# Kernel optimization log

Measured on AMD Instinct MI355X. Metric: run time of the kernel, lower is better.

The kernel has to match this reference:

```python
import jax, jax.numpy as jnp
import numpy as np

B, S, D = 2, 2048, 2048          # batch, seq_len, model_dim
H, HD, RD, L = 16, 128, 64, 512  # heads, head_dim, rope_dim, latent_dim


def _rope_cos_sin(seq_len, dim, dtype):
    inv_freq = 1.0 / (10000.0 ** (jnp.arange(0, dim, 2, dtype=jnp.float32) / dim))
    freqs = jnp.outer(jnp.arange(seq_len, dtype=jnp.float32), inv_freq)  # [S, dim/2]
    emb = jnp.concatenate([freqs, freqs], axis=-1)                        # [S, dim]
    return jnp.cos(emb).astype(dtype), jnp.sin(emb).astype(dtype)


def _rotate_half(x):
    x1, x2 = jnp.split(x, 2, axis=-1)
    return jnp.concatenate([-x2, x1], axis=-1)


def _apply_rope(q, k):
    # q, k: [B, S, H, rope_dim]
    cos, sin = _rope_cos_sin(q.shape[1], q.shape[-1], q.dtype)
    cos = cos[None, :, None, :]
    sin = sin[None, :, None, :]
    return q * cos + _rotate_half(q) * sin, k * cos + _rotate_half(k) * sin


def setup_inputs() -> dict:
    key = jax.random.key(0)
    ks = jax.random.split(key, 6)
    x = jax.random.normal(ks[0], (B, S, D), dtype=jnp.float32)
    mask = jnp.tril(jnp.ones((1, 1, S, S), dtype=jnp.bool_))  # causal
    s = lambda fan_in: 1.0 / np.sqrt(fan_in)
    w_kv_down = jax.random.normal(ks[1], (D, L), jnp.float32) * s(D)
    w_kv_up = jax.random.normal(ks[2], (L, H * (2 * HD + RD)), jnp.float32) * s(L)
    w_q_down = jax.random.normal(ks[3], (D, L), jnp.float32) * s(D)
    w_q_up = jax.random.normal(ks[4], (L, H * (HD + RD)), jnp.float32) * s(L)
    w_o = jax.random.normal(ks[5], (H * HD, D), jnp.float32) * s(H * HD)
    return dict(x=x, mask=mask, w_kv_down=w_kv_down, w_kv_up=w_kv_up,
                w_q_down=w_q_down, w_q_up=w_q_up, w_o=w_o)


def reference(x, mask, w_kv_down, w_kv_up, w_q_down, w_q_up, w_o):
    b, s, _ = x.shape
    # low-rank KV path
    kv_full = (x @ w_kv_down @ w_kv_up).reshape(b, s, H, 2 * HD + RD)
    k_content = kv_full[..., :HD]
    k_rope = kv_full[..., HD:HD + RD]
    v = kv_full[..., HD + RD:]                     # [b, s, H, HD]
    # low-rank Q path
    q_full = (x @ w_q_down @ w_q_up).reshape(b, s, H, HD + RD)
    q_content = q_full[..., :HD]
    q_rope = q_full[..., HD:]
    # partial RoPE on the rope slice only
    q_rope, k_rope = _apply_rope(q_rope, k_rope)
    q = jnp.concatenate([q_content, q_rope], axis=-1)  # [b, s, H, HD+RD]
    k = jnp.concatenate([k_content, k_rope], axis=-1)
    scale = 1.0 / np.sqrt(HD + RD)
    scores = jnp.einsum('bqhd,bkhd->bhqk', q, k) * scale
    scores = jnp.where(mask, scores, jnp.finfo(scores.dtype).min)
    attn = jax.nn.softmax(scores, axis=-1)          # dropout_p=0.0 -> identity
    context = jnp.einsum('bhqk,bkhd->bqhd', attn, v).reshape(b, s, H * HD)
    return context @ w_o
```

## Files before the change

kernel.cpp:

```cpp
#include <hip/hip_runtime.h>
#include <hip/hip_bf16.h>

#define B_ 2
#define S_ 2048
#define D_ 2048
#define H_ 16
#define HD_ 128
#define RD_ 64
#define L_ 512
#define BS_ (B_ * S_)
#define KVH 320
#define QH 192

typedef unsigned short u16;
typedef __bf16 bf16x8 __attribute__((ext_vector_type(8)));
typedef float f32x4 __attribute__((ext_vector_type(4)));
typedef unsigned short us8 __attribute__((ext_vector_type(8)));
typedef unsigned short us4 __attribute__((ext_vector_type(4)));

#define MFMA16(A, B, C) __builtin_amdgcn_mfma_f32_16x16x32_bf16((A), (B), (C), 0, 0, 0)

__device__ __forceinline__ u16 f2bf(float f) {
    unsigned int u = __builtin_bit_cast(unsigned int, f);
    u += 0x7FFFu + ((u >> 16) & 1u);
    return (u16)(u >> 16);
}
__device__ __forceinline__ float bf2f(u16 u) {
    unsigned int x = ((unsigned int)u) << 16;
    return __builtin_bit_cast(float, x);
}
__device__ __forceinline__ void async16(const void* g, void* l) {
    __builtin_amdgcn_global_load_lds((void __attribute__((address_space(1)))*)g,
                                     (void __attribute__((address_space(3)))*)l, 16, 0, 0);
}
__device__ __forceinline__ int swz4(int row) { return (row + (row >> 2)) & 3; }

__global__ __launch_bounds__(256) void conv_f32_bf16(const float* __restrict__ in,
                                                     u16* __restrict__ outp) {
    const int i = blockIdx.x * 256 + threadIdx.x;
    float4 v = *(const float4*)(in + (size_t)i * 4);
    us4 o; o[0] = f2bf(v.x); o[1] = f2bf(v.y); o[2] = f2bf(v.z); o[3] = f2bf(v.w);
    *(us4*)(outp + (size_t)i * 4) = o;
}

__global__ __launch_bounds__(256) void transpose_f32_bf16(const float* __restrict__ W,
                                                          u16* __restrict__ Wt,
                                                          int K, int N) {
    __shared__ float tile[32][33];
    const int t = threadIdx.x, tx = t & 31, ty = t >> 5;
    const int n0 = blockIdx.x * 32, k0 = blockIdx.y * 32;
#pragma unroll
    for (int r = 0; r < 4; r++)
        tile[ty + 8 * r][tx] = W[(size_t)(k0 + ty + 8 * r) * N + n0 + tx];
    __syncthreads();
#pragma unroll
    for (int r = 0; r < 4; r++)
        Wt[(size_t)(n0 + ty + 8 * r) * K + k0 + tx] = f2bf(tile[tx][ty + 8 * r]);
}

__global__ __launch_bounds__(256) void transpose_v(const u16* __restrict__ kvf,
                                                   u16* __restrict__ vtg) {
    __shared__ u16 tile[32][33];
    const int t = threadIdx.x, tx = t & 31, ty = t >> 5;
    const int bh = blockIdx.z, b = bh >> 4, h = bh & 15;
    const int s0 = blockIdx.x * 32, d0 = blockIdx.y * 32;
#pragma unroll
    for (int r = 0; r < 4; r++)
        tile[ty + 8 * r][tx] = kvf[(size_t)(b * S_ + s0 + ty + 8 * r) * (H_ * KVH) + h * KVH + QH + d0 + tx];
    __syncthreads();
#pragma unroll
    for (int r = 0; r < 4; r++)
        vtg[((size_t)bh * HD_ + d0 + ty + 8 * r) * S_ + s0 + tx] = tile[tx][ty + 8 * r];
}

__global__ __launch_bounds__(256) void rope_both(u16* __restrict__ qf,
                                                 u16* __restrict__ kvf) {
    const int idx = blockIdx.x * 256 + threadIdx.x;
    const int d = idx & 31;
    const int h = (idx >> 5) & (H_ - 1);
    const int s = (idx >> 9) & (S_ - 1);
    const int b = idx >> 20;
    const int stride = blockIdx.y ? KVH : QH;
    u16* buf = blockIdx.y ? kvf : qf;

    const float inv_freq = powf(10000.0f, -(float)d * (1.0f / 32.0f));
    const float ang = (float)s * inv_freq;
    const float c = cosf(ang), sn = sinf(ang);

    u16* p = buf + ((size_t)((b * S_ + s) * H_) + h) * stride + HD_ + d;
    const float x1 = bf2f(p[0]);
    const float x2 = bf2f(p[32]);
    p[0]  = f2bf(x1 * c - x2 * sn);
    p[32] = f2bf(x2 * c + x1 * sn);
}

template <int WM, int WN, int TM, int TN, bool OUT_F32>
__global__ __launch_bounds__(WM * WN * 64) void gemm_bf16(
    const u16* __restrict__ A, int lda,
    const u16* __restrict__ Bt, int ldb,
    void* __restrict__ Cv, int ldc, int K) {
    constexpr int BMt = WM * TM * 16;
    constexpr int BNt = WN * TN * 16;
    constexpr int NW  = WM * WN;
    constexpr int CA  = BMt / 16;
    constexpr int CB  = BNt / 16;

    __shared__ u16 As[BMt * 32];
    __shared__ u16 Bs[BNt * 32];

    const int t = threadIdx.x, w = t >> 6, l = t & 63;
    const int quad = l >> 4, n16 = l & 15;
    const int wr = w / WN, wc = w % WN;
    const size_t m0 = (size_t)blockIdx.y * BMt;
    const size_t n0 = (size_t)blockIdx.x * BNt;
    const int rowc = l >> 2, sbp = l & 3;

    f32x4 acc[TM][TN];
#pragma unroll
    for (int i = 0; i < TM; i++)
#pragma unroll
        for (int j = 0; j < TN; j++) acc[i][j] = (f32x4){0.f, 0.f, 0.f, 0.f};

    for (int k0 = 0; k0 < K; k0 += 32) {
#pragma unroll
        for (int c = w; c < CA; c += NW) {
            const int row = c * 16 + rowc;
            const int colc = ((sbp - swz4(row)) & 3) * 8;
            async16(A + (m0 + row) * lda + k0 + colc, &As[c * 512 + l * 8]);
        }
#pragma unroll
        for (int c = w; c < CB; c += NW) {
            const int row = c * 16 + rowc;
            const int colc = ((sbp - swz4(row)) & 3) * 8;
            async16(Bt + (n0 + row) * ldb + k0 + colc, &Bs[c * 512 + l * 8]);
        }
        __syncthreads();

        bf16x8 af[TM], bfr[TN];
#pragma unroll
        for (int i = 0; i < TM; i++) {
            const int row = wr * TM * 16 + i * 16 + n16;
            af[i] = *(const bf16x8*)&As[row * 32 + ((quad + swz4(row)) & 3) * 8];
        }
#pragma unroll
        for (int j = 0; j < TN; j++) {
            const int row = wc * TN * 16 + j * 16 + n16;
            bfr[j] = *(const bf16x8*)&Bs[row * 32 + ((quad + swz4(row)) & 3) * 8];
        }
#pragma unroll
        for (int i = 0; i < TM; i++)
#pragma unroll
            for (int j = 0; j < TN; j++) acc[i][j] = MFMA16(af[i], bfr[j], acc[i][j]);
        __syncthreads();
    }

#pragma unroll
    for (int i = 0; i < TM; i++) {
#pragma unroll
        for (int j = 0; j < TN; j++) {
#pragma unroll
            for (int r = 0; r < 4; r++) {
                const size_t row = m0 + wr * TM * 16 + i * 16 + quad * 4 + r;
                const size_t col = n0 + wc * TN * 16 + j * 16 + n16;
                if (OUT_F32) ((float*)Cv)[row * ldc + col] = acc[i][j][r];
                else         ((u16*)Cv)[row * ldc + col] = f2bf(acc[i][j][r]);
            }
        }
    }
}

#define PST 88

__global__ __launch_bounds__(256) void attn_mfma(const u16* __restrict__ qf,
                                                 const u16* __restrict__ kvf,
                                                 const u16* __restrict__ vtg,
                                                 u16* __restrict__ ctx) {
    __shared__ u16 Ks[2][6 * 2048];
    __shared__ u16 Vs[2 * 4096];
    __shared__ u16 Ps[4][16 * PST];

    const int t = threadIdx.x, w = t >> 6, lane = t & 63;
    const int quad = lane >> 4, n16 = lane & 15;
    const int bh = blockIdx.y, b = bh >> 4, h = bh & 15;
    const int q0 = (S_ / 64 - 1 - (int)blockIdx.x) * 64;

    const float sc2 = 1.442695041f / 13.856406461f;

    const u16* Kbase = kvf + (size_t)(b * S_) * (H_ * KVH) + h * KVH;
    const u16* Vbase = vtg + (size_t)bh * HD_ * S_;

    const int srow = lane >> 2;
    const int sbp  = lane & 3;

    bf16x8 qfrag[6];
    {
        const u16* qr = qf + (size_t)(b * S_ + q0 + w * 16 + n16) * (H_ * QH) + h * QH + quad * 8;
#pragma unroll
        for (int c = 0; c < 6; c++) qfrag[c] = *(const bf16x8*)(qr + c * 32);
    }

    f32x4 O[8];
#pragma unroll
    for (int i = 0; i < 8; i++) O[i] = (f32x4){0.f, 0.f, 0.f, 0.f};
    float lrun = 0.f;

    const int nkt = q0 / 64 + 1;

#define ISSUE_K(KT, BUF)                                                          \
    _Pragma("unroll")                                                             \
    for (int i = w; i < 24; i += 4) {                                             \
        const int c = i >> 2, g = i & 3;                                          \
        const int row = g * 16 + srow;                                            \
        const int colc = ((sbp - swz4(row)) & 3) * 8;                             \
        async16(Kbase + (size_t)((KT) * 64 + row) * (H_ * KVH) + c * 32 + colc,   \
                &Ks[BUF][c * 2048 + g * 512 + lane * 8]);                         \
    }
#define ISSUE_V(KT)                                                               \
    _Pragma("unroll")                                                             \
    for (int i = w; i < 16; i += 4) {                                             \
        const int c2 = i >> 3, g = i & 7;                                         \
        const int dim = g * 16 + srow;                                            \
        const int colc = ((sbp - swz4(dim)) & 3) * 8;                             \
        async16(Vbase + (size_t)dim * S_ + (KT) * 64 + c2 * 32 + colc,            \
                &Vs[c2 * 4096 + g * 512 + lane * 8]);                             \
    }

    ISSUE_K(0, 0);
    ISSUE_V(0);

    for (int kt = 0; kt < nkt; kt++) {
        const int cur = kt & 1;
        if (kt > 0) {
            asm volatile("s_barrier" ::: "memory");
            ISSUE_V(kt);
        }
        if (kt + 1 < nkt) {
            ISSUE_K(kt + 1, cur ^ 1);
            asm volatile("s_waitcnt vmcnt(10)" ::: "memory");
        } else {
            asm volatile("s_waitcnt vmcnt(4)" ::: "memory");
        }
        asm volatile("s_barrier" ::: "memory");

        float Sv[4][4];
#pragma unroll
        for (int nt = 0; nt < 4; nt++) {
            const int row = nt * 16 + n16;
            f32x4 s = (f32x4){0.f, 0.f, 0.f, 0.f};
#pragma unroll
            for (int c = 0; c < 6; c++) {
                bf16x8 kf = *(const bf16x8*)&Ks[cur][c * 2048 + row * 32 + ((quad + swz4(row)) & 3) * 8];
                s = MFMA16(kf, qfrag[c], s);
            }
#pragma unroll
            for (int r = 0; r < 4; r++) Sv[nt][r] = s[r];
        }
        if (kt * 64 == q0) {
#pragma unroll
            for (int nt = 0; nt < 4; nt++)
#pragma unroll
                for (int r = 0; r < 4; r++)
                    if (nt * 16 + 4 * quad + r > w * 16 + n16) Sv[nt][r] = -1.0e30f;
        }

#pragma unroll
        for (int nt = 0; nt < 4; nt++) {
            us4 pk;
#pragma unroll
            for (int r = 0; r < 4; r++) {
                const float p = exp2f(Sv[nt][r] * sc2);
                lrun += p;
                pk[r] = f2bf(p);
            }
            *(us4*)&Ps[w][n16 * PST + nt * 16 + 4 * quad] = pk;
        }

        if (kt + 1 < nkt) asm volatile("s_waitcnt vmcnt(6)" ::: "memory");
        else              asm volatile("s_waitcnt vmcnt(0)" ::: "memory");
        asm volatile("s_barrier" ::: "memory");

#pragma unroll
        for (int c2 = 0; c2 < 2; c2++) {
            bf16x8 pf = *(const bf16x8*)&Ps[w][n16 * PST + c2 * 32 + 8 * quad];
#pragma unroll
            for (int nt = 0; nt < 8; nt++) {
                const int row = nt * 16 + n16;
                bf16x8 vf = *(const bf16x8*)&Vs[c2 * 4096 + row * 32 + ((quad + swz4(row)) & 3) * 8];
                O[nt] = MFMA16(pf, vf, O[nt]);
            }
        }
    }

    lrun += __shfl_xor(lrun, 16, 64);
    lrun += __shfl_xor(lrun, 32, 64);

    float inv[4];
#pragma unroll
    for (int r = 0; r < 4; r++) inv[r] = 1.0f / __shfl(lrun, 4 * quad + r, 64);

#pragma unroll
    for (int nt = 0; nt < 8; nt++)
#pragma unroll
        for (int r = 0; r < 4; r++) {
            const int qrow = q0 + w * 16 + quad * 4 + r;
            ctx[(size_t)(b * S_ + qrow) * (H_ * HD_) + h * HD_ + nt * 16 + n16] =
                f2bf(O[nt][r] * inv[r]);
        }
}

extern "C" void kernel_launch(void* const* d_in, const int* in_sizes, int n_in,
                              void* d_out, int out_size, void* d_ws, size_t ws_size,
                              hipStream_t stream) {
    const float* x         = (const float*)d_in[0];
    const float* w_kv_down = (const float*)d_in[2];
    const float* w_kv_up   = (const float*)d_in[3];
    const float* w_q_down  = (const float*)d_in[4];
    const float* w_q_up    = (const float*)d_in[5];
    const float* w_o       = (const float*)d_in[6];
    float* out = (float*)d_out;

    char* ws = (char*)d_ws;
    size_t off = 0;
    u16* xb      = (u16*)(ws + off); off += (size_t)BS_ * D_ * 2;
    u16* wdt     = (u16*)(ws + off); off += (size_t)1024 * D_ * 2;
    u16* wkvup_t = (u16*)(ws + off); off += (size_t)(H_ * KVH) * L_ * 2;
    u16* wqup_t  = (u16*)(ws + off); off += (size_t)(H_ * QH) * L_ * 2;
    u16* wo_t    = (u16*)(ws + off); off += (size_t)D_ * (H_ * HD_) * 2;
    u16* low     = (u16*)(ws + off); off += (size_t)BS_ * 1024 * 2;
    u16* kv_full = (u16*)(ws + off); off += (size_t)BS_ * H_ * KVH * 2;
    u16* q_full  = (u16*)(ws + off); off += (size_t)BS_ * H_ * QH * 2;
    u16* vtg     = (u16*)(ws + off); off += (size_t)B_ * H_ * HD_ * S_ * 2;
    u16* ctx     = (u16*)(ws + off); off += (size_t)BS_ * H_ * HD_ * 2;

    conv_f32_bf16<<<(BS_ * D_) / 1024, 256, 0, stream>>>(x, xb);
    transpose_f32_bf16<<<dim3(L_ / 32, D_ / 32), 256, 0, stream>>>(w_kv_down, wdt, D_, L_);
    transpose_f32_bf16<<<dim3(L_ / 32, D_ / 32), 256, 0, stream>>>(w_q_down, wdt + (size_t)512 * D_, D_, L_);
    transpose_f32_bf16<<<dim3((H_ * KVH) / 32, L_ / 32), 256, 0, stream>>>(w_kv_up, wkvup_t, L_, H_ * KVH);
    transpose_f32_bf16<<<dim3((H_ * QH) / 32, L_ / 32), 256, 0, stream>>>(w_q_up, wqup_t, L_, H_ * QH);
    transpose_f32_bf16<<<dim3(D_ / 32, (H_ * HD_) / 32), 256, 0, stream>>>(w_o, wo_t, H_ * HD_, D_);

    gemm_bf16<2, 2, 4, 2, false><<<dim3(1024 / 64, BS_ / 128), 256, 0, stream>>>(
        xb, D_, wdt, D_, low, 1024, D_);
    gemm_bf16<2, 2, 4, 4, false><<<dim3((H_ * KVH) / 128, BS_ / 128), 256, 0, stream>>>(
        low, 1024, wkvup_t, L_, kv_full, H_ * KVH, L_);
    gemm_bf16<2, 2, 4, 4, false><<<dim3((H_ * QH) / 128, BS_ / 128), 256, 0, stream>>>(
        low + 512, 1024, wqup_t, L_, q_full, H_ * QH, L_);

    rope_both<<<dim3((B_ * S_ * H_ * 32) / 256, 2), 256, 0, stream>>>(q_full, kv_full);

    transpose_v<<<dim3(S_ / 32, HD_ / 32, B_ * H_), 256, 0, stream>>>(kv_full, vtg);

    attn_mfma<<<dim3(S_ / 64, B_ * H_), 256, 0, stream>>>(q_full, kv_full, vtg, ctx);

    gemm_bf16<2, 2, 4, 4, true><<<dim3(D_ / 128, BS_ / 128), 256, 0, stream>>>(
        ctx, D_, wo_t, D_, out, D_, D_);
}
```

Baseline: 455.1 us.

## Rewrite attention kernel with 32x32 MFMA, register-resident P, and XCD-aware scheduling

The attention kernel now handles 128 query rows per block with each wave owning 32 rows, and uses 32x32x16 MFMA for both QK^T and PV. The probability tile is packed with v_cvt_pk_bf16_f32 and rearranged via permlane32_swap so it stays in registers instead of round-tripping through LDS. It also changes the LDS swizzle to XOR-based, remaps a 1D grid so each XCD gets a fixed set of heads with balanced causal workloads, and adds s_setprio around the MFMA bursts. The intent is less LDS traffic, larger MFMA tiles and better load balance across chiplets, at the cost of higher register pressure (12 Q fragments plus 4 f32x16 accumulators) and waves that sit idle on causal tiles they do not need.

```diff
diff --git a/kernel.cpp b/kernel.cpp
--- a/kernel.cpp
+++ b/kernel.cpp
@@ -15,10 +15,12 @@
 typedef unsigned short u16;
 typedef __bf16 bf16x8 __attribute__((ext_vector_type(8)));
 typedef float f32x4 __attribute__((ext_vector_type(4)));
+typedef float f32x16 __attribute__((ext_vector_type(16)));
 typedef unsigned short us8 __attribute__((ext_vector_type(8)));
 typedef unsigned short us4 __attribute__((ext_vector_type(4)));
 
 #define MFMA16(A, B, C) __builtin_amdgcn_mfma_f32_16x16x32_bf16((A), (B), (C), 0, 0, 0)
+#define MFMA32(A, B, C) __builtin_amdgcn_mfma_f32_32x32x16_bf16((A), (B), (C), 0, 0, 0)
 
 __device__ __forceinline__ u16 f2bf(float f) {
     unsigned int u = __builtin_bit_cast(unsigned int, f);
@@ -34,6 +36,11 @@
                                      (void __attribute__((address_space(3)))*)l, 16, 0, 0);
 }
 __device__ __forceinline__ int swz4(int row) { return (row + (row >> 2)) & 3; }
+__device__ __forceinline__ unsigned int cvtpk_bf16(float lo, float hi) {
+    unsigned int r;
+    asm("v_cvt_pk_bf16_f32 %0, %1, %2" : "=v"(r) : "v"(lo), "v"(hi));
+    return r;
+}
 
 __global__ __launch_bounds__(256) void conv_f32_bf16(const float* __restrict__ in,
                                                      u16* __restrict__ outp) {
@@ -169,60 +176,65 @@
     }
 }
 
-#define PST 88
-
-__global__ __launch_bounds__(256) void attn_mfma(const u16* __restrict__ qf,
-                                                 const u16* __restrict__ kvf,
-                                                 const u16* __restrict__ vtg,
-                                                 u16* __restrict__ ctx) {
-    __shared__ u16 Ks[2][6 * 2048];
-    __shared__ u16 Vs[2 * 4096];
-    __shared__ u16 Ps[4][16 * PST];
+__global__ __launch_bounds__(256, 2) void attn_mfma(const u16* __restrict__ qf,
+                                                    const u16* __restrict__ kvf,
+                                                    const u16* __restrict__ vtg,
+                                                    u16* __restrict__ ctx) {
+    __shared__ u16 Ks[2][3 * 64 * 64];
+    __shared__ u16 Vs[128 * 64];
 
     const int t = threadIdx.x, w = t >> 6, lane = t & 63;
-    const int quad = lane >> 4, n16 = lane & 15;
-    const int bh = blockIdx.y, b = bh >> 4, h = bh & 15;
-    const int q0 = (S_ / 64 - 1 - (int)blockIdx.x) * 64;
+    const int l31 = lane & 31, hi = lane >> 5;
+
+    const int wg = blockIdx.x;
+    const int xcd = wg & 7, ii = wg >> 3;
+    const int tt = ii & 15;
+    const int pp = (tt & 1) ? (tt >> 1) : (15 - (tt >> 1));
+    const int qi = (ii & 32) ? (15 - pp) : pp;
+    const int bh = xcd + 8 * (ii >> 4);
+    const int b = bh >> 4, h = bh & 15;
+    const int Q0 = qi * 128;
 
     const float sc2 = 1.442695041f / 13.856406461f;
 
     const u16* Kbase = kvf + (size_t)(b * S_) * (H_ * KVH) + h * KVH;
     const u16* Vbase = vtg + (size_t)bh * HD_ * S_;
 
-    const int srow = lane >> 2;
-    const int sbp  = lane & 3;
-
-    bf16x8 qfrag[6];
+    const int scol = ((lane & 7) ^ (lane >> 3)) * 8;
+    const int krl  = lane >> 3;
+
+    bf16x8 qfrag[12];
     {
-        const u16* qr = qf + (size_t)(b * S_ + q0 + w * 16 + n16) * (H_ * QH) + h * QH + quad * 8;
-#pragma unroll
-        for (int c = 0; c < 6; c++) qfrag[c] = *(const bf16x8*)(qr + c * 32);
-    }
-
-    f32x4 O[8];
-#pragma unroll
-    for (int i = 0; i < 8; i++) O[i] = (f32x4){0.f, 0.f, 0.f, 0.f};
+        const u16* qr = qf + (size_t)(b * S_ + Q0 + w * 32 + l31) * (H_ * QH) + h * QH + hi * 8;
+#pragma unroll
+        for (int c = 0; c < 12; c++) qfrag[c] = *(const bf16x8*)(qr + c * 16);
+    }
+    asm volatile("" ::: "memory");
+
+    f32x16 O[4];
+#pragma unroll
+    for (int i = 0; i < 4; i++)
+#pragma unroll
+        for (int r = 0; r < 16; r++) O[i][r] = 0.f;
     float lrun = 0.f;
 
-    const int nkt = q0 / 64 + 1;
-
-#define ISSUE_K(KT, BUF)                                                          \
-    _Pragma("unroll")                                                             \
-    for (int i = w; i < 24; i += 4) {                                             \
-        const int c = i >> 2, g = i & 3;                                          \
-        const int row = g * 16 + srow;                                            \
-        const int colc = ((sbp - swz4(row)) & 3) * 8;                             \
-        async16(Kbase + (size_t)((KT) * 64 + row) * (H_ * KVH) + c * 32 + colc,   \
-                &Ks[BUF][c * 2048 + g * 512 + lane * 8]);                         \
-    }
-#define ISSUE_V(KT)                                                               \
-    _Pragma("unroll")                                                             \
-    for (int i = w; i < 16; i += 4) {                                             \
-        const int c2 = i >> 3, g = i & 7;                                         \
-        const int dim = g * 16 + srow;                                            \
-        const int colc = ((sbp - swz4(dim)) & 3) * 8;                             \
-        async16(Vbase + (size_t)dim * S_ + (KT) * 64 + c2 * 32 + colc,            \
-                &Vs[c2 * 4096 + g * 512 + lane * 8]);                             \
+    const int qg = Q0 + w * 32 + l31;
+    const int qmaxw = Q0 + w * 32 + 31;
+    const int nkt = Q0 / 64 + 2;
+
+#define ISSUE_K(KT, BUF)                                                        \
+    _Pragma("unroll")                                                           \
+    for (int ch = w; ch < 24; ch += 4) {                                        \
+        const int c3 = ch >> 3, kq = ch & 7;                                    \
+        async16(Kbase + (size_t)((KT) * 64 + kq * 8 + krl) * (H_ * KVH)         \
+                      + c3 * 64 + scol,                                         \
+                &Ks[BUF][c3 * 4096 + kq * 512 + lane * 8]);                     \
+    }
+#define ISSUE_V(KT)                                                             \
+    _Pragma("unroll")                                                           \
+    for (int ch = w; ch < 16; ch += 4) {                                        \
+        async16(Vbase + (size_t)(ch * 8 + krl) * S_ + (KT) * 64 + scol,         \
+                &Vs[ch * 512 + lane * 8]);                                      \
     }
 
     ISSUE_K(0, 0);
@@ -242,69 +254,92 @@
         }
         asm volatile("s_barrier" ::: "memory");
 
-        float Sv[4][4];
-#pragma unroll
-        for (int nt = 0; nt < 4; nt++) {
-            const int row = nt * 16 + n16;
-            f32x4 s = (f32x4){0.f, 0.f, 0.f, 0.f};
-#pragma unroll
-            for (int c = 0; c < 6; c++) {
-                bf16x8 kf = *(const bf16x8*)&Ks[cur][c * 2048 + row * 32 + ((quad + swz4(row)) & 3) * 8];
-                s = MFMA16(kf, qfrag[c], s);
-            }
-#pragma unroll
-            for (int r = 0; r < 4; r++) Sv[nt][r] = s[r];
-        }
-        if (kt * 64 == q0) {
-#pragma unroll
-            for (int nt = 0; nt < 4; nt++)
-#pragma unroll
-                for (int r = 0; r < 4; r++)
-                    if (nt * 16 + 4 * quad + r > w * 16 + n16) Sv[nt][r] = -1.0e30f;
-        }
-
-#pragma unroll
-        for (int nt = 0; nt < 4; nt++) {
-            us4 pk;
-#pragma unroll
-            for (int r = 0; r < 4; r++) {
-                const float p = exp2f(Sv[nt][r] * sc2);
-                lrun += p;
-                pk[r] = f2bf(p);
-            }
-            *(us4*)&Ps[w][n16 * PST + nt * 16 + 4 * quad] = pk;
+        const bool active = (kt * 64) <= qmaxw;
+        bf16x8 pfrag[4];
+        if (active) {
+            const int swz = (l31 & 7) * 8;
+            f32x16 sA, sB;
+#pragma unroll
+            for (int r = 0; r < 16; r++) { sA[r] = 0.f; sB[r] = 0.f; }
+            __builtin_amdgcn_s_setprio(1);
+#pragma unroll
+            for (int c = 0; c < 12; c++) {
+                const int cb = (c & 3) * 16 + hi * 8;
+                const int base = (c >> 2) * 4096 + (cb ^ swz);
+                bf16x8 kf0 = *(const bf16x8*)&Ks[cur][base + l31 * 64];
+                bf16x8 kf1 = *(const bf16x8*)&Ks[cur][base + (32 + l31) * 64];
+                sA = MFMA32(kf0, qfrag[c], sA);
+                sB = MFMA32(kf1, qfrag[c], sB);
+            }
+            __builtin_amdgcn_s_setprio(0);
+
+            const bool diag = (kt * 64 + 63) > (Q0 + w * 32);
+#pragma unroll
+            for (int r = 0; r < 16; r++) {
+                const int crow = (r & 3) + 8 * (r >> 2) + 4 * hi;
+                float pa = exp2f(sA[r] * sc2);
+                float pb = exp2f(sB[r] * sc2);
+                if (diag) {
+                    if (kt * 64 + crow > qg) pa = 0.f;
+                    if (kt * 64 + 32 + crow > qg) pb = 0.f;
+                }
+                lrun += pa + pb;
+                sA[r] = pa;
+                sB[r] = pb;
+            }
+
+#pragma unroll
+            for (int s = 0; s < 4; s++) {
+                const f32x16 src = (s < 2) ? sA : sB;
+                const int r0 = (s & 1) * 8;
+                unsigned int x0 = cvtpk_bf16(src[r0 + 0], src[r0 + 1]);
+                unsigned int y0 = cvtpk_bf16(src[r0 + 4], src[r0 + 5]);
+                unsigned int x1 = cvtpk_bf16(src[r0 + 2], src[r0 + 3]);
+                unsigned int y1 = cvtpk_bf16(src[r0 + 6], src[r0 + 7]);
+                asm volatile("v_permlane32_swap_b32 %0, %1" : "+v"(x0), "+v"(y0));
+                asm volatile("v_permlane32_swap_b32 %0, %1" : "+v"(x1), "+v"(y1));
+                union { unsigned int wv[4]; bf16x8 v; } u;
+                u.wv[0] = x0; u.wv[1] = x1; u.wv[2] = y0; u.wv[3] = y1;
+                pfrag[s] = u.v;
+            }
         }
 
         if (kt + 1 < nkt) asm volatile("s_waitcnt vmcnt(6)" ::: "memory");
         else              asm volatile("s_waitcnt vmcnt(0)" ::: "memory");
         asm volatile("s_barrier" ::: "memory");
 
-#pragma unroll
-        for (int c2 = 0; c2 < 2; c2++) {
-            bf16x8 pf = *(const bf16x8*)&Ps[w][n16 * PST + c2 * 32 + 8 * quad];
-#pragma unroll
-            for (int nt = 0; nt < 8; nt++) {
-                const int row = nt * 16 + n16;
-                bf16x8 vf = *(const bf16x8*)&Vs[c2 * 4096 + row * 32 + ((quad + swz4(row)) & 3) * 8];
-                O[nt] = MFMA16(pf, vf, O[nt]);
-            }
-        }
-    }
-
-    lrun += __shfl_xor(lrun, 16, 64);
+        if (active) {
+            __builtin_amdgcn_s_setprio(1);
+#pragma unroll
+            for (int s = 0; s < 4; s++) {
+#pragma unroll
+                for (int dt = 0; dt < 4; dt++) {
+                    const int d = dt * 32 + l31;
+                    bf16x8 vf = *(const bf16x8*)&Vs[d * 64 + ((s * 16 + hi * 8) ^ ((d & 7) * 8))];
+                    O[dt] = MFMA32(pfrag[s], vf, O[dt]);
+                }
+            }
+            __builtin_amdgcn_s_setprio(0);
+        }
+    }
+#undef ISSUE_K
+#undef ISSUE_V
+
     lrun += __shfl_xor(lrun, 32, 64);
-
-    float inv[4];
-#pragma unroll
-    for (int r = 0; r < 4; r++) inv[r] = 1.0f / __shfl(lrun, 4 * quad + r, 64);
-
-#pragma unroll
-    for (int nt = 0; nt < 8; nt++)
-#pragma unroll
-        for (int r = 0; r < 4; r++) {
-            const int qrow = q0 + w * 16 + quad * 4 + r;
-            ctx[(size_t)(b * S_ + qrow) * (H_ * HD_) + h * HD_ + nt * 16 + n16] =
-                f2bf(O[nt][r] * inv[r]);
+    float inv[16];
+#pragma unroll
+    for (int r = 0; r < 16; r++) {
+        const int crow = (r & 3) + 8 * (r >> 2) + 4 * hi;
+        inv[r] = 1.0f / __shfl(lrun, crow, 64);
+    }
+#pragma unroll
+    for (int dt = 0; dt < 4; dt++)
+#pragma unroll
+        for (int r = 0; r < 16; r++) {
+            const int crow = (r & 3) + 8 * (r >> 2) + 4 * hi;
+            const int qrow = Q0 + w * 32 + crow;
+            ctx[(size_t)(b * S_ + qrow) * (H_ * HD_) + h * HD_ + dt * 32 + l31] =
+                f2bf(O[dt][r] * inv[r]);
         }
 }
 
@@ -350,7 +385,7 @@
 
     transpose_v<<<dim3(S_ / 32, HD_ / 32, B_ * H_), 256, 0, stream>>>(kv_full, vtg);
 
-    attn_mfma<<<dim3(S_ / 64, B_ * H_), 256, 0, stream>>>(q_full, kv_full, vtg, ctx);
+    attn_mfma<<<dim3(512), 256, 0, stream>>>(q_full, kv_full, vtg, ctx);
 
     gemm_bf16<2, 2, 4, 4, true><<<dim3(D_ / 128, BS_ / 128), 256, 0, stream>>>(
         ctx, D_, wo_t, D_, out, D_, D_);
```

After: 399.3 us. 12.2% less time.
